# Kernel optimization log

Measured on AMD Instinct MI355X. Metric: run time of the kernel, lower is better.

Reference implementation:

```python
import jax, jax.numpy as jnp
import numpy as np

N_NODES = 50000
N_EDGES = 800000
IN_FEATS = 128
HIDDEN = 128
NUM_CLASSES = 47


def setup_inputs() -> dict:
    key = jax.random.key(0)
    k1, k2, k3, k4 = jax.random.split(key, 4)
    features = jax.random.normal(k1, (N_NODES, IN_FEATS), dtype=jnp.float32)
    edge_index = jax.random.randint(k2, (2, N_EDGES), 0, N_NODES, dtype=jnp.int32)
    # Glorot-style init for weights, zeros for bias (DGL GraphConv defaults)
    W1 = jax.random.normal(k3, (IN_FEATS, HIDDEN), dtype=jnp.float32) * (1.0 / np.sqrt(IN_FEATS))
    b1 = jnp.zeros((HIDDEN,), dtype=jnp.float32)
    W2 = jax.random.normal(k4, (HIDDEN, NUM_CLASSES), dtype=jnp.float32) * (1.0 / np.sqrt(HIDDEN))
    b2 = jnp.zeros((NUM_CLASSES,), dtype=jnp.float32)
    return {"features": features, "edge_index": edge_index,
            "W1": W1, "b1": b1, "W2": W2, "b2": b2}


def _graph_conv(x, W, b, src, dst, norm_src, norm_dst, n_nodes):
    # DGL GraphConv, norm='both': D_dst^{-1/2} A D_src^{-1/2} (X W) + b
    h = (x * norm_src[:, None]) @ W            # transform before aggregation
    agg = jax.ops.segment_sum(h[src], dst, num_segments=n_nodes)
    return agg * norm_dst[:, None] + b


def reference(features, edge_index, W1, b1, W2, b2):
    src, dst = edge_index[0], edge_index[1]
    n = features.shape[0]
    ones = jnp.ones((src.shape[0],), dtype=features.dtype)
    deg_out = jax.ops.segment_sum(ones, src, num_segments=n)
    deg_in = jax.ops.segment_sum(ones, dst, num_segments=n)
    norm_src = jax.lax.rsqrt(jnp.clip(deg_out, 1.0))   # d_out^{-1/2}, clamp >= 1
    norm_dst = jax.lax.rsqrt(jnp.clip(deg_in, 1.0))    # d_in^{-1/2}, clamp >= 1

    h = _graph_conv(features, W1, b1, src, dst, norm_src, norm_dst, n)
    h = jax.nn.relu(h)
    out = _graph_conv(h, W2, b2, src, dst, norm_src, norm_dst, n)
    return out
```

## Files before the change

### kernel.cpp

```cpp
#include <hip/hip_runtime.h>
#include <hip/hip_fp16.h>

#define N_NODES 50000
#define N_EDGES 800000
#define IN_F 128
#define HID 128
#define NCLS 47
#define H2S 48
#define W2C 64
#define NCH 196
#define NB 64
#define CHUNK 12500
#define PDW 12500
#define HHALF 6250
#define FQ 3125
#define NHIST 256
#define GROWS 128


typedef _Float16 f16x8 __attribute__((ext_vector_type(8)));
typedef float f32x4 __attribute__((ext_vector_type(4)));

struct __align__(8)  h2x2 { __half2 a, b; };
struct __align__(16) h2x4 { __half2 a, b, c, d; };

__global__ __launch_bounds__(512) void hist_kernel(const int* __restrict__ ei,
                                                   unsigned int* __restrict__ Pdst,
                                                   unsigned int* __restrict__ Psrc) {
    __shared__ unsigned int h[HHALF];
    const int t = threadIdx.x;
    const int job = blockIdx.x;
    const bool is_src = job >= NHIST / 2;
    const int half = (job >> 6) & 1;
    const int chunk = job & (NB - 1);
    const int* ids = is_src ? ei : ei + N_EDGES;
    uint2* h2 = (uint2*)h;
    for (int j = t; j < HHALF / 2; j += 512) h2[j] = make_uint2(0u, 0u);
    __syncthreads();
    const int e0 = chunk * CHUNK;
    const int lo = half * HHALF;
    for (int k = t; k < CHUNK; k += 512) {
        int v = ids[e0 + k];
        int rel = (v >> 2) - lo;
        if ((unsigned)rel < HHALF)
            atomicAdd(&h[rel], 1u << ((v & 3) * 8));
    }
    __syncthreads();
    unsigned int* P = (is_src ? Psrc : Pdst) + (size_t)chunk * PDW + lo;
    uint2* P2 = (uint2*)P;
    for (int j = t; j < HHALF / 2; j += 512) P2[j] = h2[j];
}

__global__ __launch_bounds__(256) void reduce_kernel(unsigned int* __restrict__ Pdst,
                                                     const unsigned int* __restrict__ Psrc,
                                                     int* __restrict__ cnt_in,
                                                     float* __restrict__ norm_src,
                                                     float* __restrict__ norm_dst,
                                                     int* __restrict__ chunk_sums) {
    __shared__ int sm[256];
    const int t = threadIdx.x;
    const int j = blockIdx.x * 256 + t;
    int tot = 0;
    if (j < PDW) {
        unsigned int run = 0;
        for (int b = 0; b < NB; ++b) {
            unsigned int v = Pdst[(size_t)b * PDW + j];
            Pdst[(size_t)b * PDW + j] = run;
            run += v;
        }
        int n0 = run & 0xff, n1 = (run >> 8) & 0xff;
        int n2 = (run >> 16) & 0xff, n3 = (run >> 24) & 0xff;
        *(int4*)&cnt_in[4 * j] = make_int4(n0, n1, n2, n3);
        *(float4*)&norm_dst[4 * j] = make_float4(
            rsqrtf(fmaxf((float)n0, 1.0f)), rsqrtf(fmaxf((float)n1, 1.0f)),
            rsqrtf(fmaxf((float)n2, 1.0f)), rsqrtf(fmaxf((float)n3, 1.0f)));
        tot = n0 + n1 + n2 + n3;
        unsigned int rs = 0;
        for (int b = 0; b < NB; ++b) rs += Psrc[(size_t)b * PDW + j];
        int s0 = rs & 0xff, s1 = (rs >> 8) & 0xff;
        int s2 = (rs >> 16) & 0xff, s3 = (rs >> 24) & 0xff;
        *(float4*)&norm_src[4 * j] = make_float4(
            rsqrtf(fmaxf((float)s0, 1.0f)), rsqrtf(fmaxf((float)s1, 1.0f)),
            rsqrtf(fmaxf((float)s2, 1.0f)), rsqrtf(fmaxf((float)s3, 1.0f)));
    }
    sm[t] = tot;
    __syncthreads();
    const int g = t & 63;
    for (int off = 32; off > 0; off >>= 1) {
        if (g < off) sm[t] += sm[t + off];
        __syncthreads();
    }
    if (g == 0) chunk_sums[blockIdx.x * 4 + (t >> 6)] = sm[t];
}

__global__ __launch_bounds__(256) void scan3_kernel(const int* __restrict__ cnt_in,
                                                    const int* __restrict__ chunk_sums,
                                                    int* __restrict__ offsets,
                                                    const float* __restrict__ W1,
                                                    const float* __restrict__ W2,
                                                    __half* __restrict__ W1Th,
                                                    __half* __restrict__ W1Tl,
                                                    __half* __restrict__ W2Th,
                                                    __half* __restrict__ W2Tl) {
    __shared__ int sm[256];
    const int t = threadIdx.x;
    int v = (t < NCH) ? chunk_sums[t] : 0;
    sm[t] = v;
    __syncthreads();
    for (int off = 1; off < 256; off <<= 1) {
        int u = (t >= off) ? sm[t - off] : 0;
        __syncthreads();
        sm[t] += u;
        __syncthreads();
    }
    const int basev = (blockIdx.x == 0) ? 0 : sm[blockIdx.x - 1];
    __syncthreads();
    const int idx = blockIdx.x * 256 + t;
    int c = (idx < N_NODES) ? cnt_in[idx] : 0;
    sm[t] = c;
    __syncthreads();
    for (int off = 1; off < 256; off <<= 1) {
        int u = (t >= off) ? sm[t - off] : 0;
        __syncthreads();
        sm[t] += u;
        __syncthreads();
    }
    if (idx < N_NODES) offsets[idx] = basev + sm[t] - c;
    if (blockIdx.x == 0) {
        if (t == 0) offsets[N_NODES] = N_EDGES;
        for (int i2 = t; i2 < W2C * HID; i2 += 256) {
            int cc = i2 >> 7, k = i2 & 127;
            float w = (cc < NCLS) ? W2[k * NCLS + cc] : 0.f;
            __half h = __float2half_rn(w);
            W2Th[i2] = h;
            W2Tl[i2] = __float2half_rn(w - __half2float(h));
        }
    }
    if (blockIdx.x == 1) {
        for (int i2 = t; i2 < IN_F * HID; i2 += 256) {
            int cc = i2 >> 7, k = i2 & 127;
            float w = W1[k * HID + cc];
            __half h = __float2half_rn(w);
            W1Th[i2] = h;
            W1Tl[i2] = __float2half_rn(w - __half2float(h));
        }
    }
}

__global__ __launch_bounds__(256) void fill_gemm1_kernel(const int* __restrict__ src,
        const int* __restrict__ dst, const int* __restrict__ offsets,
        const unsigned int* __restrict__ Pdst, int* __restrict__ csr_src,
        const float* __restrict__ X, const __half* __restrict__ W1Th,
        const __half* __restrict__ W1Tl, __half* __restrict__ H1h) {
    __shared__ __align__(16) unsigned int cur[FQ];
    const int t = threadIdx.x;
    if (blockIdx.x < 4 * NB) {
        const int quarter = blockIdx.x >> 6;
        const int chunk = blockIdx.x & (NB - 1);
        for (int j = t; j < FQ; j += 256) cur[j] = 0u;
        __syncthreads();
        const unsigned int* base = Pdst + (size_t)chunk * PDW;
        const int e0 = chunk * CHUNK;
        const int lo = quarter * FQ;
        for (int k = t; k < CHUNK; k += 256) {
            int d = dst[e0 + k];
            int rel = (d >> 2) - lo;
            if ((unsigned)rel < FQ) {
                const int sh = (d & 3) * 8;
                unsigned int old = atomicAdd(&cur[rel], 1u << sh);
                unsigned int rank = (old >> sh) & 0xffu;
                unsigned int bh = (base[d >> 2] >> sh) & 0xffu;
                csr_src[offsets[d] + (int)bh + (int)rank] = src[e0 + k];
            }
        }
    } else {
        const int lane = t & 63;
        const int wv = t >> 6;
        const int r16 = lane & 15;
        const int kg = lane >> 4;
        const int row0 = (blockIdx.x - 4 * NB) * GROWS + wv * 32;
        f32x4 acc[2][8] = {};
#pragma unroll
        for (int s = 0; s < 4; ++s) {
            const int k0 = 32 * s + 8 * kg;
            f16x8 ah[2], al[2];
#pragma unroll
            for (int rt = 0; rt < 2; ++rt) {
                int row = row0 + rt * 16 + r16;
                int rc = row < N_NODES ? row : N_NODES - 1;
                const float4 x0 = *(const float4*)&X[(size_t)rc * IN_F + k0];
                const float4 x1 = *(const float4*)&X[(size_t)rc * IN_F + k0 + 4];
                const float xv[8] = {x0.x, x0.y, x0.z, x0.w,
                                     x1.x, x1.y, x1.z, x1.w};
#pragma unroll
                for (int j = 0; j < 8; ++j) {
                    _Float16 h = (_Float16)xv[j];
                    ah[rt][j] = h;
                    al[rt][j] = (_Float16)(xv[j] - (float)h);
                }
            }
#pragma unroll
            for (int tt = 0; tt < 8; ++tt) {
                const f16x8 bh = *(const f16x8*)&W1Th[(16 * tt + r16) * IN_F + k0];
                const f16x8 bl = *(const f16x8*)&W1Tl[(16 * tt + r16) * IN_F + k0];
#pragma unroll
                for (int rt = 0; rt < 2; ++rt) {
                    acc[rt][tt] = __builtin_amdgcn_mfma_f32_16x16x32_f16(
                        ah[rt], bh, acc[rt][tt], 0, 0, 0);
                    acc[rt][tt] = __builtin_amdgcn_mfma_f32_16x16x32_f16(
                        al[rt], bh, acc[rt][tt], 0, 0, 0);
                    acc[rt][tt] = __builtin_amdgcn_mfma_f32_16x16x32_f16(
                        ah[rt], bl, acc[rt][tt], 0, 0, 0);
                }
            }
        }
#pragma unroll
        for (int rt = 0; rt < 2; ++rt)
#pragma unroll
            for (int j = 0; j < 4; ++j) {
                const int row = row0 + rt * 16 + 4 * kg + j;
                if (row < N_NODES) {
#pragma unroll
                    for (int tt = 0; tt < 8; ++tt)
                        H1h[(size_t)row * HID + 16 * tt + r16] =
                            __float2half_rn(acc[rt][tt][j]);
                }
            }
    }
}

__global__ __launch_bounds__(256) void gather1_kernel(const __half* __restrict__ H1h,
        const int* __restrict__ offsets, const int* __restrict__ csr_src,
        const float* __restrict__ b1, const float* __restrict__ norm_src,
        const float* __restrict__ norm_dst, __half* __restrict__ Hrelu16) {
    const int lane = threadIdx.x & 63;
    const int q = lane >> 4;
    const int fl = lane & 15;
    const int row = blockIdx.x * 4 + (threadIdx.x >> 6);
    const int beg = offsets[row], end = offsets[row + 1];
    float a0 = 0.f, a1 = 0.f, a2 = 0.f, a3 = 0.f;
    float a4 = 0.f, a5 = 0.f, a6 = 0.f, a7 = 0.f;
    for (int base = beg; base < end; base += 64) {
        int idx = 0;
        float nsv = 0.f;
        if (base + lane < end) {
            idx = csr_src[base + lane];
            nsv = norm_src[idx];
        }
        const int cnt = min(end - base, 64);
        for (int j = 0; j < cnt; j += 16) {
            int e0 = j + q, e1 = j + 4 + q, e2 = j + 8 + q, e3 = j + 12 + q;
            int s0 = __shfl(idx, e0);  float n0 = __shfl(nsv, e0);
            int s1 = __shfl(idx, e1);  float n1 = __shfl(nsv, e1);
            int s2 = __shfl(idx, e2);  float n2 = __shfl(nsv, e2);
            int s3 = __shfl(idx, e3);  float n3 = __shfl(nsv, e3);
            h2x4 v0 = *(const h2x4*)&H1h[(size_t)s0 * HID + 8 * fl];
            h2x4 v1 = *(const h2x4*)&H1h[(size_t)s1 * HID + 8 * fl];
            h2x4 v2 = *(const h2x4*)&H1h[(size_t)s2 * HID + 8 * fl];
            h2x4 v3 = *(const h2x4*)&H1h[(size_t)s3 * HID + 8 * fl];
            float2 f;
            f = __half22float2(v0.a); a0 = fmaf(f.x, n0, a0); a1 = fmaf(f.y, n0, a1);
            f = __half22float2(v0.b); a2 = fmaf(f.x, n0, a2); a3 = fmaf(f.y, n0, a3);
            f = __half22float2(v0.c); a4 = fmaf(f.x, n0, a4); a5 = fmaf(f.y, n0, a5);
            f = __half22float2(v0.d); a6 = fmaf(f.x, n0, a6); a7 = fmaf(f.y, n0, a7);
            f = __half22float2(v1.a); a0 = fmaf(f.x, n1, a0); a1 = fmaf(f.y, n1, a1);
            f = __half22float2(v1.b); a2 = fmaf(f.x, n1, a2); a3 = fmaf(f.y, n1, a3);
            f = __half22float2(v1.c); a4 = fmaf(f.x, n1, a4); a5 = fmaf(f.y, n1, a5);
            f = __half22float2(v1.d); a6 = fmaf(f.x, n1, a6); a7 = fmaf(f.y, n1, a7);
            f = __half22float2(v2.a); a0 = fmaf(f.x, n2, a0); a1 = fmaf(f.y, n2, a1);
            f = __half22float2(v2.b); a2 = fmaf(f.x, n2, a2); a3 = fmaf(f.y, n2, a3);
            f = __half22float2(v2.c); a4 = fmaf(f.x, n2, a4); a5 = fmaf(f.y, n2, a5);
            f = __half22float2(v2.d); a6 = fmaf(f.x, n2, a6); a7 = fmaf(f.y, n2, a7);
            f = __half22float2(v3.a); a0 = fmaf(f.x, n3, a0); a1 = fmaf(f.y, n3, a1);
            f = __half22float2(v3.b); a2 = fmaf(f.x, n3, a2); a3 = fmaf(f.y, n3, a3);
            f = __half22float2(v3.c); a4 = fmaf(f.x, n3, a4); a5 = fmaf(f.y, n3, a5);
            f = __half22float2(v3.d); a6 = fmaf(f.x, n3, a6); a7 = fmaf(f.y, n3, a7);
        }
    }
    a0 += __shfl_xor(a0, 16); a1 += __shfl_xor(a1, 16);
    a2 += __shfl_xor(a2, 16); a3 += __shfl_xor(a3, 16);
    a4 += __shfl_xor(a4, 16); a5 += __shfl_xor(a5, 16);
    a6 += __shfl_xor(a6, 16); a7 += __shfl_xor(a7, 16);
    a0 += __shfl_xor(a0, 32); a1 += __shfl_xor(a1, 32);
    a2 += __shfl_xor(a2, 32); a3 += __shfl_xor(a3, 32);
    a4 += __shfl_xor(a4, 32); a5 += __shfl_xor(a5, 32);
    a6 += __shfl_xor(a6, 32); a7 += __shfl_xor(a7, 32);
    if (lane < 16) {
        float nd = norm_dst[row], ns = norm_src[row];
        float4 bA = *(const float4*)&b1[8 * fl];
        float4 bB = *(const float4*)&b1[8 * fl + 4];
        float o0 = fmaxf(fmaf(a0, nd, bA.x), 0.f) * ns;
        float o1 = fmaxf(fmaf(a1, nd, bA.y), 0.f) * ns;
        float o2 = fmaxf(fmaf(a2, nd, bA.z), 0.f) * ns;
        float o3 = fmaxf(fmaf(a3, nd, bA.w), 0.f) * ns;
        float o4 = fmaxf(fmaf(a4, nd, bB.x), 0.f) * ns;
        float o5 = fmaxf(fmaf(a5, nd, bB.y), 0.f) * ns;
        float o6 = fmaxf(fmaf(a6, nd, bB.z), 0.f) * ns;
        float o7 = fmaxf(fmaf(a7, nd, bB.w), 0.f) * ns;
        h2x4 p = {__floats2half2_rn(o0, o1), __floats2half2_rn(o2, o3),
                  __floats2half2_rn(o4, o5), __floats2half2_rn(o6, o7)};
        *(h2x4*)&Hrelu16[(size_t)row * HID + 8 * fl] = p;
    }
}

__global__ __launch_bounds__(256) void gemm2_kernel(const __half* __restrict__ Hrelu16,
                                                    const __half* __restrict__ W2Th,
                                                    const __half* __restrict__ W2Tl,
                                                    __half* __restrict__ H2h) {
    const int lane = threadIdx.x & 63;
    const int wv = threadIdx.x >> 6;
    const int r16 = lane & 15;
    const int kg = lane >> 4;
    const int row0 = blockIdx.x * GROWS + wv * 32;
    f32x4 acc[2][3] = {};
#pragma unroll
    for (int s = 0; s < 4; ++s) {
        const int k0 = 32 * s + 8 * kg;
        f16x8 a[2];
#pragma unroll
        for (int rt = 0; rt < 2; ++rt) {
            int row = row0 + rt * 16 + r16;
            int rc = row < N_NODES ? row : N_NODES - 1;
            a[rt] = *(const f16x8*)&Hrelu16[(size_t)rc * HID + k0];
        }
#pragma unroll
        for (int tt = 0; tt < 3; ++tt) {
            const f16x8 bh = *(const f16x8*)&W2Th[(16 * tt + r16) * HID + k0];
            const f16x8 bl = *(const f16x8*)&W2Tl[(16 * tt + r16) * HID + k0];
#pragma unroll
            for (int rt = 0; rt < 2; ++rt) {
                acc[rt][tt] = __builtin_amdgcn_mfma_f32_16x16x32_f16(
                    a[rt], bh, acc[rt][tt], 0, 0, 0);
                acc[rt][tt] = __builtin_amdgcn_mfma_f32_16x16x32_f16(
                    a[rt], bl, acc[rt][tt], 0, 0, 0);
            }
        }
    }
#pragma unroll
    for (int rt = 0; rt < 2; ++rt)
#pragma unroll
        for (int j = 0; j < 4; ++j) {
            const int row = row0 + rt * 16 + 4 * kg + j;
            if (row < N_NODES) {
#pragma unroll
                for (int tt = 0; tt < 3; ++tt)
                    H2h[(size_t)row * H2S + 16 * tt + r16] =
                        __float2half_rn(acc[rt][tt][j]);
            }
        }
}

__global__ __launch_bounds__(256) void gather2_kernel(const __half* __restrict__ H2h,
        const int* __restrict__ offsets, const int* __restrict__ csr_src,
        const float* __restrict__ b2, const float* __restrict__ norm_dst,
        float* __restrict__ out) {
    const int lane = threadIdx.x & 63;
    const int row = blockIdx.x * 4 + (threadIdx.x >> 6);
    const int beg = offsets[row], end = offsets[row + 1];
    const int cl = min(lane, H2S - 1);
    float acc = 0.f;
    for (int base = beg; base < end; base += 64) {
        int idx = 0;
        float wv = 0.f;
        if (base + lane < end) {
            idx = csr_src[base + lane];
            wv = 1.f;
        }
        const int cnt = min(end - base, 64);
        for (int j = 0; j < cnt; j += 4) {
            int s0 = __shfl(idx, j);     float w0 = __shfl(wv, j);
            int s1 = __shfl(idx, j + 1); float w1 = __shfl(wv, j + 1);
            int s2 = __shfl(idx, j + 2); float w2 = __shfl(wv, j + 2);
            int s3 = __shfl(idx, j + 3); float w3 = __shfl(wv, j + 3);
            float f0 = __half2float(H2h[(size_t)s0 * H2S + cl]);
            float f1 = __half2float(H2h[(size_t)s1 * H2S + cl]);
            float f2 = __half2float(H2h[(size_t)s2 * H2S + cl]);
            float f3 = __half2float(H2h[(size_t)s3 * H2S + cl]);
            acc = fmaf(f0, w0, acc);
            acc = fmaf(f1, w1, acc);
            acc = fmaf(f2, w2, acc);
            acc = fmaf(f3, w3, acc);
        }
    }
    if (lane < NCLS) out[(size_t)row * NCLS + lane] = acc * norm_dst[row] + b2[lane];
}

extern "C" void kernel_launch(void* const* d_in, const int* in_sizes, int n_in,
                              void* d_out, int out_size, void* d_ws, size_t ws_size,
                              hipStream_t stream) {
    const float* X  = (const float*)d_in[0];
    const int*   ei = (const int*)d_in[1];
    const float* W1 = (const float*)d_in[2];
    const float* b1 = (const float*)d_in[3];
    const float* W2 = (const float*)d_in[4];
    const float* b2 = (const float*)d_in[5];
    float* out = (float*)d_out;

    const int* src = ei;
    const int* dst = ei + N_EDGES;

    char* w = (char*)d_ws;
    auto alloc = [&](size_t bytes) {
        char* p = w;
        w += (bytes + 255) & ~(size_t)255;
        return p;
    };
    float*  norm_src   = (float*)alloc(N_NODES * 4);
    float*  norm_dst   = (float*)alloc(N_NODES * 4);
    int*    cnt_in     = (int*)alloc(N_NODES * 4);
    int*    offsets    = (int*)alloc((N_NODES + 1) * 4);
    int*    csr_src    = (int*)alloc((size_t)N_EDGES * 4);
    int*    chunk_sums = (int*)alloc(NCH * 4);
    __half* W1Th       = (__half*)alloc((size_t)IN_F * HID * 2);
    __half* W1Tl       = (__half*)alloc((size_t)IN_F * HID * 2);
    __half* W2Th       = (__half*)alloc((size_t)W2C * HID * 2);
    __half* W2Tl       = (__half*)alloc((size_t)W2C * HID * 2);
    __half* H1h        = (__half*)alloc((size_t)N_NODES * HID * 2);
    __half* Hrelu16    = (__half*)alloc((size_t)N_NODES * HID * 2);
    __half* H2h        = (__half*)alloc((size_t)N_NODES * H2S * 2);
    unsigned int* Pdst = (unsigned int*)alloc((size_t)NB * PDW * 4);
    unsigned int* Psrc = (unsigned int*)alloc((size_t)NB * PDW * 4);

    const int gemm_blocks = (N_NODES + GROWS - 1) / GROWS;
    hist_kernel<<<NHIST, 512, 0, stream>>>(ei, Pdst, Psrc);
    reduce_kernel<<<(PDW + 255) / 256, 256, 0, stream>>>(Pdst, Psrc, cnt_in,
                                                         norm_src, norm_dst, chunk_sums);
    scan3_kernel<<<NCH, 256, 0, stream>>>(cnt_in, chunk_sums, offsets,
                                          W1, W2, W1Th, W1Tl, W2Th, W2Tl);
    fill_gemm1_kernel<<<4 * NB + gemm_blocks, 256, 0, stream>>>(src, dst, offsets,
                                                                Pdst, csr_src,
                                                                X, W1Th, W1Tl, H1h);
    gather1_kernel<<<N_NODES / 4, 256, 0, stream>>>(H1h, offsets, csr_src, b1,
                                                    norm_src, norm_dst, Hrelu16);
    gemm2_kernel<<<gemm_blocks, 256, 0, stream>>>(Hrelu16, W2Th, W2Tl, H2h);
    gather2_kernel<<<N_NODES / 4, 256, 0, stream>>>(H2h, offsets, csr_src, b2,
                                                    norm_dst, out);
}
```

Baseline: 204.6 us.

## Double histogram chunks, vectorize edge loads, move weight split into hist kernel

```diff
diff --git a/kernel.cpp b/kernel.cpp
--- a/kernel.cpp
+++ b/kernel.cpp
@@ -9,13 +9,14 @@
 #define H2S 48
 #define W2C 64
 #define NCH 196
-#define NB 64
-#define CHUNK 12500
+#define NB 128
+#define CHUNK 6250
 #define PDW 12500
 #define HHALF 6250
 #define FQ 3125
-#define NHIST 256
-#define GROWS 128
+#define NHIST 512
+#define G1ROWS 256
+#define G2ROWS 128
 
 
 typedef _Float16 f16x8 __attribute__((ext_vector_type(8)));
@@ -26,12 +27,38 @@
 
 __global__ __launch_bounds__(512) void hist_kernel(const int* __restrict__ ei,
                                                    unsigned int* __restrict__ Pdst,
-                                                   unsigned int* __restrict__ Psrc) {
+                                                   unsigned int* __restrict__ Psrc,
+                                                   const float* __restrict__ W1,
+                                                   const float* __restrict__ W2,
+                                                   __half* __restrict__ W1Th,
+                                                   __half* __restrict__ W1Tl,
+                                                   __half* __restrict__ W2Th,
+                                                   __half* __restrict__ W2Tl) {
     __shared__ unsigned int h[HHALF];
     const int t = threadIdx.x;
     const int job = blockIdx.x;
+    if (job >= NHIST) {
+        if (job == NHIST) {
+            for (int i2 = t; i2 < W2C * HID; i2 += 512) {
+                int cc = i2 >> 7, k = i2 & 127;
+                float w = (cc < NCLS) ? W2[k * NCLS + cc] : 0.f;
+                __half hv = __float2half_rn(w);
+                W2Th[i2] = hv;
+                W2Tl[i2] = __float2half_rn(w - __half2float(hv));
+            }
+        } else {
+            for (int i2 = t; i2 < IN_F * HID; i2 += 512) {
+                int cc = i2 >> 7, k = i2 & 127;
+                float w = W1[k * HID + cc];
+                __half hv = __float2half_rn(w);
+                W1Th[i2] = hv;
+                W1Tl[i2] = __float2half_rn(w - __half2float(hv));
+            }
+        }
+        return;
+    }
     const bool is_src = job >= NHIST / 2;
-    const int half = (job >> 6) & 1;
+    const int half = (job >> 7) & 1;
     const int chunk = job & (NB - 1);
     const int* ids = is_src ? ei : ei + N_EDGES;
     uint2* h2 = (uint2*)h;
@@ -39,11 +66,13 @@
     __syncthreads();
     const int e0 = chunk * CHUNK;
     const int lo = half * HHALF;
-    for (int k = t; k < CHUNK; k += 512) {
-        int v = ids[e0 + k];
-        int rel = (v >> 2) - lo;
-        if ((unsigned)rel < HHALF)
-            atomicAdd(&h[rel], 1u << ((v & 3) * 8));
+    const int2* e2p = (const int2*)(ids + e0);
+    for (int k = t; k < CHUNK / 2; k += 512) {
+        int2 v2 = e2p[k];
+        int r0 = (v2.x >> 2) - lo;
+        if ((unsigned)r0 < HHALF) atomicAdd(&h[r0], 1u << ((v2.x & 3) * 8));
+        int r1 = (v2.y >> 2) - lo;
+        if ((unsigned)r1 < HHALF) atomicAdd(&h[r1], 1u << ((v2.y & 3) * 8));
     }
     __syncthreads();
     unsigned int* P = (is_src ? Psrc : Pdst) + (size_t)chunk * PDW + lo;
@@ -63,6 +92,7 @@
     int tot = 0;
     if (j < PDW) {
         unsigned int run = 0;
+#pragma unroll 8
         for (int b = 0; b < NB; ++b) {
             unsigned int v = Pdst[(size_t)b * PDW + j];
             Pdst[(size_t)b * PDW + j] = run;
@@ -76,6 +106,7 @@
             rsqrtf(fmaxf((float)n2, 1.0f)), rsqrtf(fmaxf((float)n3, 1.0f)));
         tot = n0 + n1 + n2 + n3;
         unsigned int rs = 0;
+#pragma unroll 8
         for (int b = 0; b < NB; ++b) rs += Psrc[(size_t)b * PDW + j];
         int s0 = rs & 0xff, s1 = (rs >> 8) & 0xff;
         int s2 = (rs >> 16) & 0xff, s3 = (rs >> 24) & 0xff;
@@ -95,13 +126,7 @@
 
 __global__ __launch_bounds__(256) void scan3_kernel(const int* __restrict__ cnt_in,
                                                     const int* __restrict__ chunk_sums,
-                                                    int* __restrict__ offsets,
-                                                    const float* __restrict__ W1,
-                                                    const float* __restrict__ W2,
-                                                    __half* __restrict__ W1Th,
-                                                    __half* __restrict__ W1Tl,
-                                                    __half* __restrict__ W2Th,
-                                                    __half* __restrict__ W2Tl) {
+                                                    int* __restrict__ offsets) {
     __shared__ int sm[256];
     const int t = threadIdx.x;
     int v = (t < NCH) ? chunk_sums[t] : 0;
@@ -126,28 +151,10 @@
         __syncthreads();
     }
     if (idx < N_NODES) offsets[idx] = basev + sm[t] - c;
-    if (blockIdx.x == 0) {
-        if (t == 0) offsets[N_NODES] = N_EDGES;
-        for (int i2 = t; i2 < W2C * HID; i2 += 256) {
-            int cc = i2 >> 7, k = i2 & 127;
-            float w = (cc < NCLS) ? W2[k * NCLS + cc] : 0.f;
-            __half h = __float2half_rn(w);
-            W2Th[i2] = h;
-            W2Tl[i2] = __float2half_rn(w - __half2float(h));
-        }
-    }
-    if (blockIdx.x == 1) {
-        for (int i2 = t; i2 < IN_F * HID; i2 += 256) {
-            int cc = i2 >> 7, k = i2 & 127;
-            float w = W1[k * HID + cc];
-            __half h = __float2half_rn(w);
-            W1Th[i2] = h;
-            W1Tl[i2] = __float2half_rn(w - __half2float(h));
-        }
-    }
-}
-
-__global__ __launch_bounds__(256) void fill_gemm1_kernel(const int* __restrict__ src,
+    if (blockIdx.x == 0 && t == 0) offsets[N_NODES] = N_EDGES;
+}
+
+__global__ __launch_bounds__(512) void fill_gemm1_kernel(const int* __restrict__ src,
         const int* __restrict__ dst, const int* __restrict__ offsets,
         const unsigned int* __restrict__ Pdst, int* __restrict__ csr_src,
         const float* __restrict__ X, const __half* __restrict__ W1Th,
@@ -155,22 +162,33 @@
     __shared__ __align__(16) unsigned int cur[FQ];
     const int t = threadIdx.x;
     if (blockIdx.x < 4 * NB) {
-        const int quarter = blockIdx.x >> 6;
+        const int quarter = blockIdx.x >> 7;
         const int chunk = blockIdx.x & (NB - 1);
-        for (int j = t; j < FQ; j += 256) cur[j] = 0u;
+        for (int j = t; j < FQ; j += 512) cur[j] = 0u;
         __syncthreads();
         const unsigned int* base = Pdst + (size_t)chunk * PDW;
         const int e0 = chunk * CHUNK;
         const int lo = quarter * FQ;
-        for (int k = t; k < CHUNK; k += 256) {
-            int d = dst[e0 + k];
-            int rel = (d >> 2) - lo;
-            if ((unsigned)rel < FQ) {
-                const int sh = (d & 3) * 8;
-                unsigned int old = atomicAdd(&cur[rel], 1u << sh);
+        const int2* d2p = (const int2*)(dst + e0);
+        const int2* s2p = (const int2*)(src + e0);
+        for (int k = t; k < CHUNK / 2; k += 512) {
+            int2 d2 = d2p[k];
+            int2 s2 = s2p[k];
+            int r0 = (d2.x >> 2) - lo;
+            if ((unsigned)r0 < FQ) {
+                const int sh = (d2.x & 3) * 8;
+                unsigned int old = atomicAdd(&cur[r0], 1u << sh);
                 unsigned int rank = (old >> sh) & 0xffu;
-                unsigned int bh = (base[d >> 2] >> sh) & 0xffu;
-                csr_src[offsets[d] + (int)bh + (int)rank] = src[e0 + k];
+                unsigned int bh = (base[d2.x >> 2] >> sh) & 0xffu;
+                csr_src[offsets[d2.x] + (int)bh + (int)rank] = s2.x;
+            }
+            int r1 = (d2.y >> 2) - lo;
+            if ((unsigned)r1 < FQ) {
+                const int sh = (d2.y & 3) * 8;
+                unsigned int old = atomicAdd(&cur[r1], 1u << sh);
+                unsigned int rank = (old >> sh) & 0xffu;
+                unsigned int bh = (base[d2.y >> 2] >> sh) & 0xffu;
+                csr_src[offsets[d2.y] + (int)bh + (int)rank] = s2.y;
             }
         }
     } else {
@@ -178,7 +196,7 @@
         const int wv = t >> 6;
         const int r16 = lane & 15;
         const int kg = lane >> 4;
-        const int row0 = (blockIdx.x - 4 * NB) * GROWS + wv * 32;
+        const int row0 = (blockIdx.x - 4 * NB) * G1ROWS + wv * 32;
         f32x4 acc[2][8] = {};
 #pragma unroll
         for (int s = 0; s < 4; ++s) {
@@ -194,9 +212,9 @@
                                      x1.x, x1.y, x1.z, x1.w};
 #pragma unroll
                 for (int j = 0; j < 8; ++j) {
-                    _Float16 h = (_Float16)xv[j];
-                    ah[rt][j] = h;
-                    al[rt][j] = (_Float16)(xv[j] - (float)h);
+                    _Float16 hv = (_Float16)xv[j];
+                    ah[rt][j] = hv;
+                    al[rt][j] = (_Float16)(xv[j] - (float)hv);
                 }
             }
 #pragma unroll
@@ -311,7 +329,7 @@
     const int wv = threadIdx.x >> 6;
     const int r16 = lane & 15;
     const int kg = lane >> 4;
-    const int row0 = blockIdx.x * GROWS + wv * 32;
+    const int row0 = blockIdx.x * G2ROWS + wv * 32;
     f32x4 acc[2][3] = {};
 #pragma unroll
     for (int s = 0; s < 4; ++s) {
@@ -421,18 +439,19 @@
     unsigned int* Pdst = (unsigned int*)alloc((size_t)NB * PDW * 4);
     unsigned int* Psrc = (unsigned int*)alloc((size_t)NB * PDW * 4);
 
-    const int gemm_blocks = (N_NODES + GROWS - 1) / GROWS;
-    hist_kernel<<<NHIST, 512, 0, stream>>>(ei, Pdst, Psrc);
+    const int g1_blocks = (N_NODES + G1ROWS - 1) / G1ROWS;
+    const int g2_blocks = (N_NODES + G2ROWS - 1) / G2ROWS;
+    hist_kernel<<<NHIST + 2, 512, 0, stream>>>(ei, Pdst, Psrc, W1, W2,
+                                               W1Th, W1Tl, W2Th, W2Tl);
     reduce_kernel<<<(PDW + 255) / 256, 256, 0, stream>>>(Pdst, Psrc, cnt_in,
                                                          norm_src, norm_dst, chunk_sums);
-    scan3_kernel<<<NCH, 256, 0, stream>>>(cnt_in, chunk_sums, offsets,
-                                          W1, W2, W1Th, W1Tl, W2Th, W2Tl);
-    fill_gemm1_kernel<<<4 * NB + gemm_blocks, 256, 0, stream>>>(src, dst, offsets,
-                                                                Pdst, csr_src,
-                                                                X, W1Th, W1Tl, H1h);
+    scan3_kernel<<<NCH, 256, 0, stream>>>(cnt_in, chunk_sums, offsets);
+    fill_gemm1_kernel<<<4 * NB + g1_blocks, 512, 0, stream>>>(src, dst, offsets,
+                                                              Pdst, csr_src,
+                                                              X, W1Th, W1Tl, H1h);
     gather1_kernel<<<N_NODES / 4, 256, 0, stream>>>(H1h, offsets, csr_src, b1,
                                                     norm_src, norm_dst, Hrelu16);
-    gemm2_kernel<<<gemm_blocks, 256, 0, stream>>>(Hrelu16, W2Th, W2Tl, H2h);
+    gemm2_kernel<<<g2_blocks, 256, 0, stream>>>(Hrelu16, W2Th, W2Tl, H2h);
     gather2_kernel<<<N_NODES / 4, 256, 0, stream>>>(H2h, offsets, csr_src, b2,
                                                     norm_dst, out);
 }
```

Result: no change. 204.0 us (-0.3%).
